# Optimization experiments

Measured on AMD Instinct MI355X. Metric: run time of the kernel, lower is better.

Reference implementation:

```python
import jax, jax.numpy as jnp
import numpy as np
from jax.scipy.special import i0

B, P = 2, 524288
N = (512, 512)            # uniform frequency grid
M = 4                     # window cutoff m (2M taps per dim)
SIGMA = 2.0
NGRID = tuple(2 * (int(SIGMA * Ni) // 2) for Ni in N)  # oversampled grid (1024, 1024)
BETA = tuple(float(np.pi * (2.0 - 1.0 / (ng / Ni))) for ng, Ni in zip(NGRID, N))


def _phi_hat_1d(Ni, ni, b):
    # Fourier coefficients of the Kaiser-Bessel window, k = -Ni/2 .. Ni/2-1
    k = jnp.arange(-Ni // 2, Ni // 2, dtype=jnp.float32)
    arg = jnp.sqrt(b * b - (2.0 * jnp.pi * k / ni) ** 2)
    return i0(M * arg) / ni


def _window_ft():
    # separable d-dim Fourier coefficient grid, shape [N1, N2] (== window.ft)
    c1 = _phi_hat_1d(N[0], NGRID[0], BETA[0])
    c2 = _phi_hat_1d(N[1], NGRID[1], BETA[1])
    return c1[:, None] * c2[None, :]


def _phi(t, ni, b):
    # Kaiser-Bessel window in time domain, support |t| <= M/ni
    u2 = M * M - (ni * t) ** 2
    u = jnp.sqrt(jnp.maximum(u2, 1e-12))
    return jnp.where(u2 > 0, jnp.sinh(b * u) / (jnp.pi * u), 0.0)


def setup_inputs() -> dict:
    key = jax.random.key(0)
    k1, k2 = jax.random.split(key)
    x = jax.random.uniform(k1, (B, P, 2), jnp.float32, -0.5, 0.5)  # points on torus
    f_hat = jax.random.normal(k2, (B, N[0], N[1], 2), jnp.float32)  # complex as [re,im]
    return {"x": x, "f_hat": f_hat}


def _nfft_forward(x, f_hat):
    # f(x_j) ~= sum_k f_hat[k] exp(-2 pi i <k, x_j>) via window-deconvolved oversampled FFT + local gather
    fh = (f_hat[..., 0] + 1j * f_hat[..., 1]).astype(jnp.complex64)  # [B, N1, N2]
    ft = _window_ft().astype(jnp.float32)
    gh = fh / ft                                                    # deconvolve
    p1 = (NGRID[0] - N[0]) // 2
    p2 = (NGRID[1] - N[1]) // 2
    gh = jnp.pad(gh, ((0, 0), (p1, p1), (p2, p2)))                  # centered zero-pad to n
    g = jnp.fft.fftn(jnp.fft.ifftshift(gh, axes=(-2, -1)), axes=(-2, -1))
    g = g / (NGRID[0] * NGRID[1])                                   # g_l = (1/n) sum_k gh_k e^{-2pi i kl/n}

    offs = jnp.arange(-M + 1, M + 1)                                # [2M]
    ws, idxs = [], []
    for d in range(2):
        nd = NGRID[d]
        xd = x[..., d]                                              # [B, P]
        l0 = jnp.floor(xd * nd).astype(jnp.int32)
        l = l0[..., None] + offs                                    # [B, P, 2M]
        t = xd[..., None] - l.astype(jnp.float32) / nd
        ws.append(_phi(t, nd, BETA[d]))
        idxs.append(jnp.mod(l, nd))

    g_flat = g.reshape(B, NGRID[0] * NGRID[1])
    acc = jnp.zeros((B, P), jnp.complex64)
    for i in range(2 * M):                                          # fixed 2m x 2m taps
        for j in range(2 * M):
            flat = idxs[0][..., i] * NGRID[1] + idxs[1][..., j]     # [B, P]
            gv = jnp.take_along_axis(g_flat, flat, axis=1)
            acc = acc + (ws[0][..., i] * ws[1][..., j]) * gv
    return jnp.stack([acc.real, acc.imag], axis=-1)                 # [B, P, 2]


def reference(x, f_hat):
    return _nfft_forward(x, f_hat)
```

## Files before the change

kernel.cpp:

```cpp
#include <hip/hip_runtime.h>

constexpr int   NGRID = 1024;
constexpr int   BATCH = 2;
constexpr int   NPTS  = 524288;
constexpr int   BINS  = 2048;
constexpr int   CAP   = 768;
constexpr float BETA  = 4.71238898038469f;
constexpr float PI_F  = 3.14159265358979f;

#define PIDX(i) ((i) + ((i) >> 4))

constexpr size_t G_BYTES  = (size_t)BATCH * NGRID * NGRID * sizeof(float2);
constexpr size_t GCNT_OFF = G_BYTES;
constexpr size_t PERM_OFF = G_BYTES + 8192;

__device__ __forceinline__ float i0f_large(float x) {
    float t = 3.75f / x;
    float p =  0.00392377f;
    p = p * t + -0.01647633f;
    p = p * t +  0.02635537f;
    p = p * t + -0.02057706f;
    p = p * t +  0.00916281f;
    p = p * t + -0.00157565f;
    p = p * t +  0.00225319f;
    p = p * t +  0.01328592f;
    p = p * t +  0.39894228f;
    return __expf(x) * rsqrtf(x) * p;
}

__device__ __forceinline__ int tile_of(float2 xv, int b) {
    int c1 = ((int)floorf(xv.x * 1024.0f)) & 1023;
    int c2 = ((int)floorf(xv.y * 1024.0f)) & 1023;
    return (b << 10) + ((c1 >> 5) << 5) + (c2 >> 5);
}

__device__ __forceinline__ float2 cmul(float2 a, float2 w) {
    return make_float2(a.x * w.x - a.y * w.y, a.x * w.y + a.y * w.x);
}

__device__ __forceinline__ int digitrev4_10(int f) {
    unsigned r = __brev((unsigned)f) >> 22;
    return (int)(((r & 0x2AAu) >> 1) | ((r & 0x155u) << 1));
}

__global__ __launch_bounds__(1024) void bin_kernel(const float2* __restrict__ x,
                                                   int* __restrict__ gcnt,
                                                   int* __restrict__ perm) {
    __shared__ int h[BINS];
    int tid = threadIdx.x;
    h[tid] = 0; h[tid + 1024] = 0;
    __syncthreads();

    int base = blockIdx.x * 8192;
    int tile[8];
    #pragma unroll
    for (int i = 0; i < 8; ++i) {
        int gid = base + tid + i * 1024;
        tile[i] = tile_of(x[gid], gid >> 19);
        atomicAdd(&h[tile[i]], 1);
    }
    __syncthreads();

    int c0 = h[tid], c1 = h[tid + 1024];
    int b0 = c0 ? atomicAdd(&gcnt[tid], c0) : 0;
    int b1 = c1 ? atomicAdd(&gcnt[tid + 1024], c1) : 0;
    __syncthreads();
    h[tid] = b0; h[tid + 1024] = b1;
    __syncthreads();

    #pragma unroll
    for (int i = 0; i < 8; ++i) {
        int pos = atomicAdd(&h[tile[i]], 1);
        perm[tile[i] * CAP + pos] = base + tid + i * 1024;
    }
}

__device__ __forceinline__ void build_tw4(float2* T, int tid, int nthreads) {
    int off = 0, q = 256, sig = 1;
    #pragma unroll
    for (int st = 0; st < 5; ++st) {
        for (int m = tid; m < 3 * q; m += nthreads) {
            int sec = 0, j = m;
            if (j >= q) { sec++; j -= q; }
            if (j >= q) { sec++; j -= q; }
            float ang = (-2.0f * PI_F / 1024.0f) * (float)((sec + 1) * j * sig);
            float sw, cw;
            __sincosf(ang, &sw, &cw);
            T[off + m] = make_float2(cw, sw);
        }
        off += 3 * q; q >>= 2; sig <<= 2;
    }
}

__device__ __forceinline__ void bfly4(float2* s, const float2* T,
                                      int bt, int q, int off) {
    int j    = bt & (q - 1);
    int base = ((bt - j) << 2) + j;
    int p0 = PIDX(base), p1 = PIDX(base + q);
    int p2 = PIDX(base + 2 * q), p3 = PIDX(base + 3 * q);
    float2 a0 = s[p0], a1 = s[p1], a2 = s[p2], a3 = s[p3];
    float2 t0 = make_float2(a0.x + a2.x, a0.y + a2.y);
    float2 t1 = make_float2(a0.x - a2.x, a0.y - a2.y);
    float2 t2 = make_float2(a1.x + a3.x, a1.y + a3.y);
    float2 t3 = make_float2(a1.x - a3.x, a1.y - a3.y);
    float2 b0 = make_float2(t0.x + t2.x, t0.y + t2.y);
    float2 b2 = make_float2(t0.x - t2.x, t0.y - t2.y);
    float2 b1 = make_float2(t1.x + t3.y, t1.y - t3.x);
    float2 b3 = make_float2(t1.x - t3.y, t1.y + t3.x);
    s[p0] = b0;
    s[p1] = cmul(b1, T[off + j]);
    s[p2] = cmul(b2, T[off + q + j]);
    s[p3] = cmul(b3, T[off + 2 * q + j]);
}

__global__ __launch_bounds__(256) void fft_rows(const float2* __restrict__ fh,
                                                float2* __restrict__ g) {
    __shared__ float2 s[1087];
    __shared__ float2 T[1023];
    int blk = blockIdx.x;
    int row = (blk < 256) ? blk : blk + 512;
    int b = blockIdx.y;
    int a1 = (row + 256) & 1023;
    int tid = threadIdx.x;

    build_tw4(T, tid, 256);

    float k1 = (float)(a1 - 256);
    float w1 = (2.0f * PI_F / 1024.0f) * k1;
    float c1 = i0f_large(4.0f * sqrtf(BETA * BETA - w1 * w1));

    const float2* fr = fh + ((long)b << 18) + ((long)a1 << 9);

    float w2a = (2.0f * PI_F / 1024.0f) * (float)tid;
    float c2a = i0f_large(4.0f * sqrtf(BETA * BETA - w2a * w2a));
    float w2b = (2.0f * PI_F / 1024.0f) * (float)(tid - 256);
    float c2b = i0f_large(4.0f * sqrtf(BETA * BETA - w2b * w2b));

    float2 va = fr[tid + 256];
    float2 vb = fr[tid];
    float ia = 1.0f / (c1 * c2a);
    float ib = 1.0f / (c1 * c2b);
    s[PIDX(tid)]       = make_float2(va.x * ia, va.y * ia);
    s[PIDX(tid + 256)] = make_float2(0.f, 0.f);
    s[PIDX(tid + 512)] = make_float2(0.f, 0.f);
    s[PIDX(tid + 768)] = make_float2(vb.x * ib, vb.y * ib);

    int off = 0, q = 256;
    #pragma unroll
    for (int st = 0; st < 5; ++st) {
        __syncthreads();
        bfly4(s, T, tid, q, off);
        off += 3 * q; q >>= 2;
    }
    __syncthreads();

    float2* base = g + ((long)b << 20) + ((long)row << 10);
    #pragma unroll
    for (int i = 0; i < 4; ++i) {
        int idx = tid + (i << 8);
        base[idx] = s[PIDX(digitrev4_10(idx))];
    }
}

__global__ __launch_bounds__(256) void fft_cols(float2* __restrict__ g) {
    constexpr int STR = 1092;
    __shared__ float2 s[4 * STR];
    __shared__ float2 T[1023];
    int b  = blockIdx.y;
    int C0 = blockIdx.x * 4;
    int t  = threadIdx.x;
    int c  = t & 3, L = t >> 2;
    float2* gb = g + ((long)b << 20);

    build_tw4(T, t, 256);

    float2* sf = s + c * STR;
    #pragma unroll
    for (int i = 0; i < 4; ++i) {
        int r = L + i * 64;
        sf[PIDX(r)] = gb[((long)r << 10) + C0 + c];
    }
    #pragma unroll
    for (int i = 0; i < 4; ++i) {
        int r = L + i * 64 + 768;
        sf[PIDX(r)] = gb[((long)r << 10) + C0 + c];
    }
    #pragma unroll
    for (int i = 0; i < 8; ++i) {
        int r = L + i * 64 + 256;
        sf[PIDX(r)] = make_float2(0.f, 0.f);
    }

    int off = 0, q = 256;
    #pragma unroll
    for (int st = 0; st < 5; ++st) {
        __syncthreads();
        #pragma unroll
        for (int rr = 0; rr < 4; ++rr)
            bfly4(sf, T, L + rr * 64, q, off);
        off += 3 * q; q >>= 2;
    }
    __syncthreads();

    #pragma unroll
    for (int i = 0; i < 16; ++i) {
        int r = L + i * 64;
        gb[((long)r << 10) + C0 + c] = sf[PIDX(digitrev4_10(r))];
    }
}

__global__ __launch_bounds__(256) void gather_binned(const float2* __restrict__ x,
                                                     const float2* __restrict__ g,
                                                     const int* __restrict__ gcnt,
                                                     const int* __restrict__ perm,
                                                     float2* __restrict__ out) {
    __shared__ float2 patch[37 * 37];
    int tb = blockIdx.x;
    int b  = tb >> 10;
    int tt = tb & 1023;
    int tR = tt >> 5, tC = tt & 31;
    int R0 = (tR << 5) - 2, C0 = (tC << 5) - 2;
    const float2* gb = g + ((long)b << 20);

    for (int p = threadIdx.x; p < 37 * 37; p += 256) {
        int pr = p / 37, pc = p - pr * 37;
        int gr = (R0 + pr) & 1023, gc = (C0 + pc) & 1023;
        patch[p] = gb[(gr << 10) + gc];
    }
    __syncthreads();

    int cnt = gcnt[tb];
    if (cnt > CAP) cnt = CAP;
    int off0 = tb * CAP;
    for (int i = (int)threadIdx.x; i < cnt; i += 256) {
        int gid = perm[off0 + i];
        float2 xv = x[gid];

        float w1[6], w2[6];
        int rr0, cc0;
        {
            float xs = xv.x * 1024.0f;
            float fl = floorf(xs);
            float fr = xs - fl;
            rr0 = (((int)fl) & 1023) - (tR << 5);
            #pragma unroll
            for (int k = 0; k < 6; ++k) {
                float tv = fr - (float)(k - 2);
                float u2 = 16.0f - tv * tv;
                float ir = rsqrtf(u2);
                float z  = BETA * u2 * ir;
                w1[k] = __expf(z) * 0.159154943f * ir;
            }
        }
        {
            float xs = xv.y * 1024.0f;
            float fl = floorf(xs);
            float fr = xs - fl;
            cc0 = (((int)fl) & 1023) - (tC << 5);
            #pragma unroll
            for (int k = 0; k < 6; ++k) {
                float tv = fr - (float)(k - 2);
                float u2 = 16.0f - tv * tv;
                float ir = rsqrtf(u2);
                float z  = BETA * u2 * ir;
                w2[k] = __expf(z) * 0.159154943f * ir;
            }
        }

        float ar = 0.0f, ai = 0.0f;
        #pragma unroll
        for (int ii = 0; ii < 6; ++ii) {
            int pbase = (rr0 + ii) * 37 + cc0;
            float wi = w1[ii];
            #pragma unroll
            for (int jj = 0; jj < 6; ++jj) {
                float2 gv = patch[pbase + jj];
                float w = wi * w2[jj];
                ar = fmaf(w, gv.x, ar);
                ai = fmaf(w, gv.y, ai);
            }
        }
        out[gid] = make_float2(ar, ai);
    }
}

extern "C" void kernel_launch(void* const* d_in, const int* in_sizes, int n_in,
                              void* d_out, int out_size, void* d_ws, size_t ws_size,
                              hipStream_t stream) {
    const float2* x  = (const float2*)d_in[0];
    const float2* fh = (const float2*)d_in[1];
    char* ws = (char*)d_ws;
    float2* g   = (float2*)ws;
    int* gcnt   = (int*)(ws + GCNT_OFF);
    int* perm   = (int*)(ws + PERM_OFF);

    hipMemsetAsync(gcnt, 0, BINS * sizeof(int), stream);
    bin_kernel<<<dim3((BATCH * NPTS) / 8192), dim3(1024), 0, stream>>>(x, gcnt, perm);

    fft_rows<<<dim3(512, BATCH), dim3(256), 0, stream>>>(fh, g);
    fft_cols<<<dim3(256, BATCH), dim3(256), 0, stream>>>(g);

    gather_binned<<<dim3(BINS), dim3(256), 0, stream>>>(x, g, gcnt, perm, (float2*)d_out);
}
```

Baseline: 126.6 us.

## Merge point binning into row FFT kernel as extra independent blocks

The separate binning kernel is folded into the row-FFT launch. Blocks 0-1023 do row FFTs and blocks 1024-1279 do binning, with 256 threads per block and 16 points per thread. This removes one kernel launch and lets the two independent tasks run at the same time on the GPU. The binning blocks now use 256 threads instead of 1024, which changes how much work each block does and how often shared atomics contend.

```diff
diff --git a/kernel.cpp b/kernel.cpp
--- a/kernel.cpp
+++ b/kernel.cpp
@@ -41,38 +41,6 @@
 __device__ __forceinline__ int digitrev4_10(int f) {
     unsigned r = __brev((unsigned)f) >> 22;
     return (int)(((r & 0x2AAu) >> 1) | ((r & 0x155u) << 1));
-}
-
-__global__ __launch_bounds__(1024) void bin_kernel(const float2* __restrict__ x,
-                                                   int* __restrict__ gcnt,
-                                                   int* __restrict__ perm) {
-    __shared__ int h[BINS];
-    int tid = threadIdx.x;
-    h[tid] = 0; h[tid + 1024] = 0;
-    __syncthreads();
-
-    int base = blockIdx.x * 8192;
-    int tile[8];
-    #pragma unroll
-    for (int i = 0; i < 8; ++i) {
-        int gid = base + tid + i * 1024;
-        tile[i] = tile_of(x[gid], gid >> 19);
-        atomicAdd(&h[tile[i]], 1);
-    }
-    __syncthreads();
-
-    int c0 = h[tid], c1 = h[tid + 1024];
-    int b0 = c0 ? atomicAdd(&gcnt[tid], c0) : 0;
-    int b1 = c1 ? atomicAdd(&gcnt[tid + 1024], c1) : 0;
-    __syncthreads();
-    h[tid] = b0; h[tid + 1024] = b1;
-    __syncthreads();
-
-    #pragma unroll
-    for (int i = 0; i < 8; ++i) {
-        int pos = atomicAdd(&h[tile[i]], 1);
-        perm[tile[i] * CAP + pos] = base + tid + i * 1024;
-    }
 }
 
 __device__ __forceinline__ void build_tw4(float2* T, int tid, int nthreads) {
@@ -113,52 +81,88 @@
     s[p3] = cmul(b3, T[off + 2 * q + j]);
 }
 
-__global__ __launch_bounds__(256) void fft_rows(const float2* __restrict__ fh,
-                                                float2* __restrict__ g) {
-    __shared__ float2 s[1087];
-    __shared__ float2 T[1023];
-    int blk = blockIdx.x;
-    int row = (blk < 256) ? blk : blk + 512;
-    int b = blockIdx.y;
-    int a1 = (row + 256) & 1023;
+__global__ __launch_bounds__(256) void rows_and_bin(const float2* __restrict__ fh,
+                                                    float2* __restrict__ g,
+                                                    const float2* __restrict__ x,
+                                                    int* __restrict__ gcnt,
+                                                    int* __restrict__ perm) {
+    __shared__ __align__(16) char smem[16880];
     int tid = threadIdx.x;
 
-    build_tw4(T, tid, 256);
-
-    float k1 = (float)(a1 - 256);
-    float w1 = (2.0f * PI_F / 1024.0f) * k1;
-    float c1 = i0f_large(4.0f * sqrtf(BETA * BETA - w1 * w1));
-
-    const float2* fr = fh + ((long)b << 18) + ((long)a1 << 9);
-
-    float w2a = (2.0f * PI_F / 1024.0f) * (float)tid;
-    float c2a = i0f_large(4.0f * sqrtf(BETA * BETA - w2a * w2a));
-    float w2b = (2.0f * PI_F / 1024.0f) * (float)(tid - 256);
-    float c2b = i0f_large(4.0f * sqrtf(BETA * BETA - w2b * w2b));
-
-    float2 va = fr[tid + 256];
-    float2 vb = fr[tid];
-    float ia = 1.0f / (c1 * c2a);
-    float ib = 1.0f / (c1 * c2b);
-    s[PIDX(tid)]       = make_float2(va.x * ia, va.y * ia);
-    s[PIDX(tid + 256)] = make_float2(0.f, 0.f);
-    s[PIDX(tid + 512)] = make_float2(0.f, 0.f);
-    s[PIDX(tid + 768)] = make_float2(vb.x * ib, vb.y * ib);
-
-    int off = 0, q = 256;
-    #pragma unroll
-    for (int st = 0; st < 5; ++st) {
-        __syncthreads();
-        bfly4(s, T, tid, q, off);
-        off += 3 * q; q >>= 2;
-    }
-    __syncthreads();
-
-    float2* base = g + ((long)b << 20) + ((long)row << 10);
-    #pragma unroll
-    for (int i = 0; i < 4; ++i) {
-        int idx = tid + (i << 8);
-        base[idx] = s[PIDX(digitrev4_10(idx))];
+    if (blockIdx.x < 1024) {
+        float2* s = (float2*)smem;
+        float2* T = (float2*)smem + 1087;
+        int blk = blockIdx.x & 511;
+        int b   = blockIdx.x >> 9;
+        int row = (blk < 256) ? blk : blk + 512;
+        int a1  = (row + 256) & 1023;
+
+        build_tw4(T, tid, 256);
+
+        float k1 = (float)(a1 - 256);
+        float w1 = (2.0f * PI_F / 1024.0f) * k1;
+        float c1 = i0f_large(4.0f * sqrtf(BETA * BETA - w1 * w1));
+
+        const float2* fr = fh + ((long)b << 18) + ((long)a1 << 9);
+
+        float w2a = (2.0f * PI_F / 1024.0f) * (float)tid;
+        float c2a = i0f_large(4.0f * sqrtf(BETA * BETA - w2a * w2a));
+        float w2b = (2.0f * PI_F / 1024.0f) * (float)(tid - 256);
+        float c2b = i0f_large(4.0f * sqrtf(BETA * BETA - w2b * w2b));
+
+        float2 va = fr[tid + 256];
+        float2 vb = fr[tid];
+        float ia = 1.0f / (c1 * c2a);
+        float ib = 1.0f / (c1 * c2b);
+        s[PIDX(tid)]       = make_float2(va.x * ia, va.y * ia);
+        s[PIDX(tid + 256)] = make_float2(0.f, 0.f);
+        s[PIDX(tid + 512)] = make_float2(0.f, 0.f);
+        s[PIDX(tid + 768)] = make_float2(vb.x * ib, vb.y * ib);
+
+        int off = 0, q = 256;
+        #pragma unroll
+        for (int st = 0; st < 5; ++st) {
+            __syncthreads();
+            bfly4(s, T, tid, q, off);
+            off += 3 * q; q >>= 2;
+        }
+        __syncthreads();
+
+        float2* base = g + ((long)b << 20) + ((long)row << 10);
+        #pragma unroll
+        for (int i = 0; i < 4; ++i) {
+            int idx = tid + (i << 8);
+            base[idx] = s[PIDX(digitrev4_10(idx))];
+        }
+    } else {
+        int* h = (int*)smem;
+        int bblk = blockIdx.x - 1024;
+        for (int i = tid; i < BINS; i += 256) h[i] = 0;
+        __syncthreads();
+
+        int base = bblk * 4096;
+        int tile[16];
+        #pragma unroll
+        for (int i = 0; i < 16; ++i) {
+            int gid = base + tid + i * 256;
+            tile[i] = tile_of(x[gid], gid >> 19);
+            atomicAdd(&h[tile[i]], 1);
+        }
+        __syncthreads();
+
+        #pragma unroll
+        for (int j = 0; j < 8; ++j) {
+            int bi = tid + j * 256;
+            int c  = h[bi];
+            h[bi]  = c ? atomicAdd(&gcnt[bi], c) : 0;
+        }
+        __syncthreads();
+
+        #pragma unroll
+        for (int i = 0; i < 16; ++i) {
+            int pos = atomicAdd(&h[tile[i]], 1);
+            perm[tile[i] * CAP + pos] = base + tid + i * 256;
+        }
     }
 }
 
@@ -295,10 +299,9 @@
     int* perm   = (int*)(ws + PERM_OFF);
 
     hipMemsetAsync(gcnt, 0, BINS * sizeof(int), stream);
-    bin_kernel<<<dim3((BATCH * NPTS) / 8192), dim3(1024), 0, stream>>>(x, gcnt, perm);
-
-    fft_rows<<<dim3(512, BATCH), dim3(256), 0, stream>>>(fh, g);
-    fft_cols<<<dim3(256, BATCH), dim3(256), 0, stream>>>(g);
+
+    rows_and_bin<<<dim3(1280), dim3(256), 0, stream>>>(fh, g, x, gcnt, perm);
+    fft_cols    <<<dim3(256, BATCH), dim3(256), 0, stream>>>(g);
 
     gather_binned<<<dim3(BINS), dim3(256), 0, stream>>>(x, g, gcnt, perm, (float2*)d_out);
 }
```

Result: faster. 123.6 us (-2.4%).
